# Kernel optimization log

Hardware: AMD Instinct MI355X
Metric: run time of the kernel (lower is better)

## Reference

```python
import jax, jax.numpy as jnp
import numpy as np

N_HEADS = 16

def setup_inputs() -> dict:
    key = jax.random.key(0)
    ks = jax.random.split(key, 5)
    B, N, D = 2, 2048, 1024
    return {
        "x": jax.random.normal(ks[0], (B, N, D), dtype=jnp.float32),
        "w_qkv": jax.random.normal(ks[1], (D, 3 * D), dtype=jnp.float32) * (1.0 / np.sqrt(D)),
        "b_qkv": jax.random.normal(ks[2], (3 * D,), dtype=jnp.float32) * 0.02,
        "w_out": jax.random.normal(ks[3], (D, D), dtype=jnp.float32) * (1.0 / np.sqrt(D)),
        "b_out": jax.random.normal(ks[4], (D,), dtype=jnp.float32) * 0.02,
    }

def reference(x, w_qkv, b_qkv, w_out, b_out):
    B, N, D = x.shape
    H = N_HEADS
    dk = D // H
    qkv = x @ w_qkv + b_qkv                       # (B, N, 3D)
    # NOTE: original reshapes to (B, N, H, 3*dk) then chunks -> per-head interleaved layout
    qkv = qkv.reshape(B, N, H, 3 * dk).transpose(2, 0, 1, 3)  # (H, B, N, 3*dk)
    q, k, v = jnp.split(qkv, 3, axis=-1)          # each (H, B, N, dk)
    scale = 1.0 / np.sqrt(dk).astype(np.float32)
    scores = jnp.einsum('hbnd,hbmd->hbnm', q, k) * scale  # (H, B, N, N)
    attn = jax.nn.softmax(scores, axis=-1)
    context = jnp.einsum('hbnm,hbmd->hbnd', attn, v)       # (H, B, N, dk)
    context = context.transpose(1, 2, 0, 3).reshape(B, N, D)
    attn_mean = attn.mean(axis=0).mean(axis=1)    # (B, N): mean over heads then over query dim
    out = context @ w_out + b_out
    return out, attn_mean
```

## Files before the change

### kernel.cpp

```cpp
#include <hip/hip_runtime.h>
#include <hip/hip_bf16.h>
#include <stdint.h>

#define B_ 2
#define N_ 2048
#define D_ 1024
#define H_ 16
#define DK 64

typedef __bf16 bf16x8 __attribute__((ext_vector_type(8)));
typedef short s16x4 __attribute__((ext_vector_type(4)));
typedef float f32x4 __attribute__((ext_vector_type(4)));

#define EXP2SC 0.18033688011112042f

__device__ __forceinline__ unsigned short f2bf(float f) {
    unsigned int u = __float_as_uint(f);
    u = (u + 0x7FFFu + ((u >> 16) & 1u)) >> 16;
    return (unsigned short)u;
}

__device__ __forceinline__ short2 pkbf(float a, float b) {
    __hip_bfloat162 t = __float22bfloat162_rn(float2{a, b});
    return *(short2*)&t;
}

__device__ __forceinline__ void glds16(const void* g, void* l) {
    __builtin_amdgcn_global_load_lds(
        (const __attribute__((address_space(1))) void*)g,
        (__attribute__((address_space(3))) void*)l, 16, 0, 0);
}

__global__ __launch_bounds__(256) void k_convert_x(const float* __restrict__ x,
                                                   unsigned short* __restrict__ xb, int n4) {
    int i = blockIdx.x * blockDim.x + threadIdx.x;
    int stride = gridDim.x * blockDim.x;
    const float4* x4 = (const float4*)x;
    ushort4* o4 = (ushort4*)xb;
    for (; i < n4; i += stride) {
        float4 v = x4[i];
        ushort4 o;
        o.x = f2bf(v.x); o.y = f2bf(v.y); o.z = f2bf(v.z); o.w = f2bf(v.w);
        o4[i] = o;
    }
}

__global__ __launch_bounds__(256) void k_transpose_w(const float* __restrict__ w,
                                                     unsigned short* __restrict__ wT,
                                                     int K, int C) {
    __shared__ float tile[32][33];
    int c0 = blockIdx.x * 32, k0 = blockIdx.y * 32;
    int tx = threadIdx.x, ty = threadIdx.y;
    for (int s = 0; s < 4; ++s)
        tile[ty + 8 * s][tx] = w[(size_t)(k0 + ty + 8 * s) * C + c0 + tx];
    __syncthreads();
    for (int s = 0; s < 4; ++s)
        wT[(size_t)(c0 + ty + 8 * s) * K + k0 + tx] = f2bf(tile[tx][ty + 8 * s]);
}

__global__ __launch_bounds__(256) void k_gemm_qkv(const unsigned short* __restrict__ A,
                                                  const unsigned short* __restrict__ BT,
                                                  const float* __restrict__ bias,
                                                  unsigned short* __restrict__ Cout,
                                                  int M, int Nn, int K) {
    __shared__ __attribute__((aligned(16))) unsigned short Alds[128 * 64];
    __shared__ __attribute__((aligned(16))) unsigned short Blds[128 * 64];
    int t = threadIdx.x;
    int lane = t & 63, w = t >> 6;
    int quad = lane >> 4, c = lane & 15;
    int wm = w >> 1, wn = w & 1;
    int bi = blockIdx.y, bj = blockIdx.x;
    const unsigned short* Abase = A + (size_t)(bi * 128) * K;
    const unsigned short* Bbase = BT + (size_t)(bj * 128) * K;

    f32x4 acc[4][4];
#pragma unroll
    for (int mf = 0; mf < 4; ++mf)
#pragma unroll
        for (int nf = 0; nf < 4; ++nf)
            acc[mf][nf] = (f32x4){0.f, 0.f, 0.f, 0.f};

    for (int k0 = 0; k0 < K; k0 += 64) {
        __syncthreads();
#pragma unroll
        for (int i = 0; i < 4; ++i) {
            int ch = i * 256 + t;
            int row = ch >> 3, kc = (ch & 7) ^ (row & 7);
            glds16(&Abase[(size_t)row * K + k0 + kc * 8], (char*)Alds + ch * 16);
            glds16(&Bbase[(size_t)row * K + k0 + kc * 8], (char*)Blds + ch * 16);
        }
        __syncthreads();
#pragma unroll
        for (int ks = 0; ks < 2; ++ks) {
            bf16x8 af[4], bfr[4];
#pragma unroll
            for (int mf = 0; mf < 4; ++mf)
                af[mf] = *(const bf16x8*)&Alds[(wm * 64 + mf * 16 + c) * 64 +
                                               (((ks * 4 + quad) ^ (c & 7)) * 8)];
#pragma unroll
            for (int nf = 0; nf < 4; ++nf)
                bfr[nf] = *(const bf16x8*)&Blds[(wn * 64 + nf * 16 + c) * 64 +
                                                (((ks * 4 + quad) ^ (c & 7)) * 8)];
#pragma unroll
            for (int mf = 0; mf < 4; ++mf)
#pragma unroll
                for (int nf = 0; nf < 4; ++nf)
                    acc[mf][nf] = __builtin_amdgcn_mfma_f32_16x16x32_bf16(af[mf], bfr[nf],
                                                                          acc[mf][nf], 0, 0, 0);
        }
    }

#pragma unroll
    for (int mf = 0; mf < 4; ++mf)
#pragma unroll
        for (int nf = 0; nf < 4; ++nf) {
            int j = bj * 128 + wn * 64 + nf * 16 + c;
            float bv = bias[j];
            int h = j / 192, r2 = j % 192;
            int which = r2 >> 6, d = r2 & 63;
#pragma unroll
            for (int r = 0; r < 4; ++r) {
                int i = bi * 128 + wm * 64 + mf * 16 + quad * 4 + r;
                float v = acc[mf][nf][r] + bv;
                int b = i >> 11, n = i & 2047;
                size_t dst;
                if (which < 2)
                    dst = (size_t)which * 4194304 + (((size_t)(h * 2 + b) * 2048 + n) * 64 + d);
                else
                    dst = (size_t)2 * 4194304 + (((size_t)(h * 2 + b) * 64 + d) * 2048 + n);
                Cout[dst] = f2bf(v);
            }
        }
}

__global__ __launch_bounds__(256) void k_gemm_out(const unsigned short* __restrict__ A,
                                                  const unsigned short* __restrict__ BT,
                                                  const float* __restrict__ bias,
                                                  float* __restrict__ C,
                                                  int M, int Nn, int K) {
    __shared__ __attribute__((aligned(16))) unsigned short Alds[64 * 64];
    __shared__ __attribute__((aligned(16))) unsigned short Blds[128 * 64];
    int t = threadIdx.x;
    int lane = t & 63, w = t >> 6;
    int quad = lane >> 4, c = lane & 15;
    int wm = w >> 1, wn = w & 1;
    int bi = blockIdx.y, bj = blockIdx.x;
    const unsigned short* Abase = A + (size_t)(bi * 64) * K;
    const unsigned short* Bbase = BT + (size_t)(bj * 128) * K;

    f32x4 acc[2][4];
#pragma unroll
    for (int mf = 0; mf < 2; ++mf)
#pragma unroll
        for (int nf = 0; nf < 4; ++nf)
            acc[mf][nf] = (f32x4){0.f, 0.f, 0.f, 0.f};

    for (int k0 = 0; k0 < K; k0 += 64) {
        __syncthreads();
#pragma unroll
        for (int i = 0; i < 2; ++i) {
            int ch = i * 256 + t;
            int row = ch >> 3, kc = (ch & 7) ^ (row & 7);
            glds16(&Abase[(size_t)row * K + k0 + kc * 8], (char*)Alds + ch * 16);
        }
#pragma unroll
        for (int i = 0; i < 4; ++i) {
            int ch = i * 256 + t;
            int row = ch >> 3, kc = (ch & 7) ^ (row & 7);
            glds16(&Bbase[(size_t)row * K + k0 + kc * 8], (char*)Blds + ch * 16);
        }
        __syncthreads();
#pragma unroll
        for (int ks = 0; ks < 2; ++ks) {
            bf16x8 af[2], bfr[4];
#pragma unroll
            for (int mf = 0; mf < 2; ++mf)
                af[mf] = *(const bf16x8*)&Alds[(wm * 32 + mf * 16 + c) * 64 +
                                               (((ks * 4 + quad) ^ (c & 7)) * 8)];
#pragma unroll
            for (int nf = 0; nf < 4; ++nf)
                bfr[nf] = *(const bf16x8*)&Blds[(wn * 64 + nf * 16 + c) * 64 +
                                                (((ks * 4 + quad) ^ (c & 7)) * 8)];
#pragma unroll
            for (int mf = 0; mf < 2; ++mf)
#pragma unroll
                for (int nf = 0; nf < 4; ++nf)
                    acc[mf][nf] = __builtin_amdgcn_mfma_f32_16x16x32_bf16(af[mf], bfr[nf],
                                                                          acc[mf][nf], 0, 0, 0);
        }
    }

#pragma unroll
    for (int mf = 0; mf < 2; ++mf)
#pragma unroll
        for (int nf = 0; nf < 4; ++nf) {
            int j = bj * 128 + wn * 64 + nf * 16 + c;
            float bv = bias[j];
#pragma unroll
            for (int r = 0; r < 4; ++r) {
                int i = bi * 64 + wm * 32 + mf * 16 + quad * 4 + r;
                C[(size_t)i * Nn + j] = acc[mf][nf][r] + bv;
            }
        }
}

__global__ __launch_bounds__(512) void k_attn(const unsigned short* __restrict__ Q,
                                              const unsigned short* __restrict__ Kc,
                                              const unsigned short* __restrict__ VT,
                                              unsigned short* __restrict__ ctx,
                                              float* __restrict__ lrs_out) {
    __shared__ __attribute__((aligned(16))) unsigned short lds[8192];
    unsigned short* Klds = lds;
    unsigned short* Vlds = lds + 4096;
    int t = threadIdx.x, lane = t & 63, w = t >> 6;
    int quad = lane >> 4, c = lane & 15;
    int qt = blockIdx.x, hb = blockIdx.y;
    int h = hb >> 1, b = hb & 1;
    const unsigned short* qbase = Q + (size_t)hb * 131072 + (size_t)(qt * 128 + w * 16) * 64;
    const unsigned short* kbase = Kc + (size_t)hb * 131072;
    const unsigned short* vtbase = VT + (size_t)hb * 131072;

    int srow = t >> 3, sB = t & 7;
    int sgoff = srow * 64 + ((sB ^ (srow & 7)) * 8);
    int vgoff = srow * 2048 + ((sB ^ (srow & 7)) * 8);

    bf16x8 qf[2];
#pragma unroll
    for (int ks = 0; ks < 2; ++ks)
        qf[ks] = *(const bf16x8*)&qbase[c * 64 + ks * 32 + quad * 8];

    f32x4 acc[4];
#pragma unroll
    for (int ds = 0; ds < 4; ++ds) acc[ds] = (f32x4){0.f, 0.f, 0.f, 0.f};
    float lsum = 0.f;

    for (int kb = 0; kb < 32; ++kb) {
        __syncthreads();
        glds16(&kbase[(size_t)kb * 4096 + sgoff], (char*)Klds + t * 16);
        glds16(&vtbase[(size_t)kb * 64 + vgoff], (char*)Vlds + t * 16);
        __syncthreads();

        f32x4 st[4];
#pragma unroll
        for (int ksub = 0; ksub < 4; ++ksub) st[ksub] = (f32x4){0.f, 0.f, 0.f, 0.f};
#pragma unroll
        for (int ks = 0; ks < 2; ++ks)
#pragma unroll
            for (int ksub = 0; ksub < 4; ++ksub) {
                bf16x8 kf = *(const bf16x8*)&Klds[(ksub * 16 + c) * 64 +
                                                  (((ks * 4 + quad) ^ (c & 7)) * 8)];
                st[ksub] = __builtin_amdgcn_mfma_f32_16x16x32_bf16(kf, qf[ks], st[ksub], 0, 0, 0);
            }
#pragma unroll
        for (int ksub = 0; ksub < 4; ++ksub) {
            float p0 = __builtin_amdgcn_exp2f(st[ksub][0] * EXP2SC);
            float p1 = __builtin_amdgcn_exp2f(st[ksub][1] * EXP2SC);
            float p2 = __builtin_amdgcn_exp2f(st[ksub][2] * EXP2SC);
            float p3 = __builtin_amdgcn_exp2f(st[ksub][3] * EXP2SC);
            lsum += (p0 + p1) + (p2 + p3);
            short2 lo = pkbf(p0, p1), hi = pkbf(p2, p3);
            s16x4 pf = (s16x4){lo.x, lo.y, hi.x, hi.y};
            s16x4 vf[4];
#pragma unroll
            for (int ds = 0; ds < 4; ++ds) {
                int row = ds * 16 + c;
                vf[ds] = *(const s16x4*)&Vlds[row * 64 +
                                              (((2 * ksub + (quad >> 1)) ^ (row & 7)) * 8) +
                                              (quad & 1) * 4];
            }
#pragma unroll
            for (int ds = 0; ds < 4; ++ds)
                acc[ds] = __builtin_amdgcn_mfma_f32_16x16x16bf16_1k(pf, vf[ds], acc[ds], 0, 0, 0);
        }
    }

    float v = lsum;
    v += __shfl_xor(v, 16);
    v += __shfl_xor(v, 32);
    if (lane < 16)
        lrs_out[hb * 2048 + qt * 128 + w * 16 + c] =
            -(__builtin_amdgcn_logf(v) + 15.0f);
    float linv = 1.0f / v;
    float ir[4];
#pragma unroll
    for (int r = 0; r < 4; ++r) ir[r] = __shfl(linv, quad * 4 + r);
#pragma unroll
    for (int ds = 0; ds < 4; ++ds)
#pragma unroll
        for (int r = 0; r < 4; ++r) {
            int n = qt * 128 + w * 16 + quad * 4 + r;
            ctx[((size_t)(b * 2048 + n)) * 1024 + h * 64 + ds * 16 + c] =
                f2bf(acc[ds][r] * ir[r]);
        }
}

__global__ __launch_bounds__(512) void k_amean(const unsigned short* __restrict__ Q,
                                               const unsigned short* __restrict__ Kc,
                                               const float* __restrict__ lrs,
                                               float* __restrict__ amean) {
    __shared__ __attribute__((aligned(16))) unsigned short Qlds[128 * 64];
    __shared__ float rslds[128];
    int t = threadIdx.x, lane = t & 63, w = t >> 6;
    int quad = lane >> 4, c = lane & 15;
    int kt = blockIdx.x, hb = blockIdx.y, b = hb & 1;
    const unsigned short* kbase = Kc + (size_t)hb * 131072 + (size_t)(kt * 128 + w * 16) * 64;
    const unsigned short* qbase = Q + (size_t)hb * 131072;

    bf16x8 kf[2];
#pragma unroll
    for (int ks = 0; ks < 2; ++ks)
        kf[ks] = *(const bf16x8*)&kbase[c * 64 + ks * 32 + quad * 8];

    f32x4 colacc = (f32x4){0.f, 0.f, 0.f, 0.f};

    for (int qc = 0; qc < 16; ++qc) {
        __syncthreads();
#pragma unroll
        for (int i = 0; i < 2; ++i) {
            int ch = i * 512 + t;
            int row = ch >> 3, Bs = ch & 7;
            glds16(&qbase[(size_t)qc * 8192 + row * 64 + ((Bs ^ (row & 7)) * 8)],
                   (char*)Qlds + ch * 16);
        }
        if (t < 128) rslds[t] = lrs[hb * 2048 + qc * 128 + t];
        __syncthreads();
#pragma unroll
        for (int qs = 0; qs < 8; ++qs) {
            f32x4 st = (f32x4){0.f, 0.f, 0.f, 0.f};
#pragma unroll
            for (int ks = 0; ks < 2; ++ks) {
                bf16x8 qfr = *(const bf16x8*)&Qlds[(qs * 16 + c) * 64 +
                                                   (((ks * 4 + quad) ^ (c & 7)) * 8)];
                st = __builtin_amdgcn_mfma_f32_16x16x32_bf16(kf[ks], qfr, st, 0, 0, 0);
            }
            float rv = rslds[qs * 16 + c];
#pragma unroll
            for (int r = 0; r < 4; ++r)
                colacc[r] += __builtin_amdgcn_exp2f(st[r] * EXP2SC + rv);
        }
    }
#pragma unroll
    for (int r = 0; r < 4; ++r) {
        float v = colacc[r];
        v += __shfl_xor(v, 1);
        v += __shfl_xor(v, 2);
        v += __shfl_xor(v, 4);
        v += __shfl_xor(v, 8);
        if (c == 0)
            atomicAdd(&amean[b * 2048 + kt * 128 + w * 16 + quad * 4 + r], v);
    }
}

extern "C" void kernel_launch(void* const* d_in, const int* in_sizes, int n_in,
                              void* d_out, int out_size, void* d_ws, size_t ws_size,
                              hipStream_t stream) {
    const float* x = (const float*)d_in[0];
    const float* w_qkv = (const float*)d_in[1];
    const float* b_qkv = (const float*)d_in[2];
    const float* w_out = (const float*)d_in[3];
    const float* b_out = (const float*)d_in[4];
    float* out = (float*)d_out;
    float* amean = out + 4194304;

    unsigned short* ws = (unsigned short*)d_ws;
    unsigned short* x_bf = ws;
    unsigned short* wqkvT = x_bf + 4194304;
    unsigned short* woutT = wqkvT + 3145728;
    unsigned short* q_bf = woutT + 1048576;
    unsigned short* k_bf = q_bf + 4194304;
    unsigned short* vT_bf = k_bf + 4194304;
    unsigned short* ctx_bf = vT_bf + 4194304;
    float* lrs = (float*)(ctx_bf + 4194304);

    hipMemsetAsync(amean, 0, 4096 * sizeof(float), stream);
    k_convert_x<<<2048, 256, 0, stream>>>(x, x_bf, 1048576);
    k_transpose_w<<<dim3(96, 32), dim3(32, 8), 0, stream>>>(w_qkv, wqkvT, 1024, 3072);
    k_transpose_w<<<dim3(32, 32), dim3(32, 8), 0, stream>>>(w_out, woutT, 1024, 1024);
    k_gemm_qkv<<<dim3(24, 32), 256, 0, stream>>>(x_bf, wqkvT, b_qkv, q_bf, 4096, 3072, 1024);
    k_attn<<<dim3(16, 32), 512, 0, stream>>>(q_bf, k_bf, vT_bf, ctx_bf, lrs);
    k_amean<<<dim3(16, 32), 512, 0, stream>>>(q_bf, k_bf, lrs, amean);
    k_gemm_out<<<dim3(8, 64), 256, 0, stream>>>(ctx_bf, woutT, b_out, out, 4096, 1024, 1024);
}
```

Measured before the change: 222.7 us.

## Double-buffer attention LDS loads, fuse prep kernels, fold softmax scale into Q

Merges the x conversion, both weight transposes and the amean memset into one prep kernel, removing several launches. Folds the exp2 softmax scale into Q during the QKV GEMM epilogue, so the attention and amean kernels skip one multiply per score. Double-buffers the K/V tiles in k_attn and the Q tiles in k_amean so the next tile's global-to-LDS load overlaps current compute, which doubles LDS use per block. Flattens the grid so consecutive blocks share a query/key tile index across heads, which changes block scheduling and cache locality.

```diff
diff --git a/kernel.cpp b/kernel.cpp
--- a/kernel.cpp
+++ b/kernel.cpp
@@ -31,31 +31,48 @@
         (__attribute__((address_space(3))) void*)l, 16, 0, 0);
 }
 
-__global__ __launch_bounds__(256) void k_convert_x(const float* __restrict__ x,
-                                                   unsigned short* __restrict__ xb, int n4) {
-    int i = blockIdx.x * blockDim.x + threadIdx.x;
-    int stride = gridDim.x * blockDim.x;
-    const float4* x4 = (const float4*)x;
-    ushort4* o4 = (ushort4*)xb;
-    for (; i < n4; i += stride) {
-        float4 v = x4[i];
-        ushort4 o;
-        o.x = f2bf(v.x); o.y = f2bf(v.y); o.z = f2bf(v.z); o.w = f2bf(v.w);
-        o4[i] = o;
-    }
-}
-
-__global__ __launch_bounds__(256) void k_transpose_w(const float* __restrict__ w,
-                                                     unsigned short* __restrict__ wT,
-                                                     int K, int C) {
+__global__ __launch_bounds__(256) void k_prep(const float* __restrict__ x,
+                                              unsigned short* __restrict__ xb,
+                                              const float* __restrict__ w_qkv,
+                                              unsigned short* __restrict__ wqkvT,
+                                              const float* __restrict__ w_out,
+                                              unsigned short* __restrict__ woutT,
+                                              float* __restrict__ amean) {
     __shared__ float tile[32][33];
-    int c0 = blockIdx.x * 32, k0 = blockIdx.y * 32;
-    int tx = threadIdx.x, ty = threadIdx.y;
-    for (int s = 0; s < 4; ++s)
-        tile[ty + 8 * s][tx] = w[(size_t)(k0 + ty + 8 * s) * C + c0 + tx];
-    __syncthreads();
-    for (int s = 0; s < 4; ++s)
-        wT[(size_t)(c0 + ty + 8 * s) * K + k0 + tx] = f2bf(tile[tx][ty + 8 * s]);
+    int blk = blockIdx.x, t = threadIdx.x;
+    if (blk < 1024) {
+        const float4* x4 = (const float4*)x;
+        ushort4* o4 = (ushort4*)xb;
+        int i = blk * 256 + t;
+#pragma unroll
+        for (int s = 0; s < 4; ++s, i += 262144) {
+            float4 v = x4[i];
+            ushort4 o;
+            o.x = f2bf(v.x); o.y = f2bf(v.y); o.z = f2bf(v.z); o.w = f2bf(v.w);
+            o4[i] = o;
+        }
+    } else if (blk < 4096) {
+        int idx = blk - 1024;
+        int c0 = (idx % 96) * 32, k0 = (idx / 96) * 32;
+        int tx = t & 31, ty = t >> 5;
+        for (int s = 0; s < 4; ++s)
+            tile[ty + 8 * s][tx] = w_qkv[(size_t)(k0 + ty + 8 * s) * 3072 + c0 + tx];
+        __syncthreads();
+        for (int s = 0; s < 4; ++s)
+            wqkvT[(size_t)(c0 + ty + 8 * s) * 1024 + k0 + tx] = f2bf(tile[tx][ty + 8 * s]);
+    } else if (blk < 5120) {
+        int idx = blk - 4096;
+        int c0 = (idx % 32) * 32, k0 = (idx / 32) * 32;
+        int tx = t & 31, ty = t >> 5;
+        for (int s = 0; s < 4; ++s)
+            tile[ty + 8 * s][tx] = w_out[(size_t)(k0 + ty + 8 * s) * 1024 + c0 + tx];
+        __syncthreads();
+        for (int s = 0; s < 4; ++s)
+            woutT[(size_t)(c0 + ty + 8 * s) * 1024 + k0 + tx] = f2bf(tile[tx][ty + 8 * s]);
+    } else {
+#pragma unroll
+        for (int s = 0; s < 16; ++s) amean[s * 256 + t] = 0.f;
+    }
 }
 
 __global__ __launch_bounds__(256) void k_gemm_qkv(const unsigned short* __restrict__ A,
@@ -122,6 +139,7 @@
             for (int r = 0; r < 4; ++r) {
                 int i = bi * 128 + wm * 64 + mf * 16 + quad * 4 + r;
                 float v = acc[mf][nf][r] + bv;
+                if (which == 0) v *= EXP2SC;
                 int b = i >> 11, n = i & 2047;
                 size_t dst;
                 if (which < 2)
@@ -209,12 +227,11 @@
                                               const unsigned short* __restrict__ VT,
                                               unsigned short* __restrict__ ctx,
                                               float* __restrict__ lrs_out) {
-    __shared__ __attribute__((aligned(16))) unsigned short lds[8192];
-    unsigned short* Klds = lds;
-    unsigned short* Vlds = lds + 4096;
+    __shared__ __attribute__((aligned(16))) unsigned short lds[16384];
     int t = threadIdx.x, lane = t & 63, w = t >> 6;
     int quad = lane >> 4, c = lane & 15;
-    int qt = blockIdx.x, hb = blockIdx.y;
+    int bi = blockIdx.x;
+    int hb = bi & 31, qt = bi >> 5;
     int h = hb >> 1, b = hb & 1;
     const unsigned short* qbase = Q + (size_t)hb * 131072 + (size_t)(qt * 128 + w * 16) * 64;
     const unsigned short* kbase = Kc + (size_t)hb * 131072;
@@ -229,16 +246,23 @@
     for (int ks = 0; ks < 2; ++ks)
         qf[ks] = *(const bf16x8*)&qbase[c * 64 + ks * 32 + quad * 8];
 
+    glds16(&kbase[sgoff], (char*)lds + t * 16);
+    glds16(&vtbase[vgoff], (char*)(lds + 4096) + t * 16);
+
     f32x4 acc[4];
 #pragma unroll
     for (int ds = 0; ds < 4; ++ds) acc[ds] = (f32x4){0.f, 0.f, 0.f, 0.f};
     float lsum = 0.f;
 
     for (int kb = 0; kb < 32; ++kb) {
-        __syncthreads();
-        glds16(&kbase[(size_t)kb * 4096 + sgoff], (char*)Klds + t * 16);
-        glds16(&vtbase[(size_t)kb * 64 + vgoff], (char*)Vlds + t * 16);
-        __syncthreads();
+        const unsigned short* Kb = lds + (kb & 1) * 8192;
+        const unsigned short* Vb = Kb + 4096;
+        __syncthreads();
+        if (kb < 31) {
+            unsigned short* Kn = lds + ((kb + 1) & 1) * 8192;
+            glds16(&kbase[(size_t)(kb + 1) * 4096 + sgoff], (char*)Kn + t * 16);
+            glds16(&vtbase[(size_t)(kb + 1) * 64 + vgoff], (char*)(Kn + 4096) + t * 16);
+        }
 
         f32x4 st[4];
 #pragma unroll
@@ -247,16 +271,16 @@
         for (int ks = 0; ks < 2; ++ks)
 #pragma unroll
             for (int ksub = 0; ksub < 4; ++ksub) {
-                bf16x8 kf = *(const bf16x8*)&Klds[(ksub * 16 + c) * 64 +
-                                                  (((ks * 4 + quad) ^ (c & 7)) * 8)];
+                bf16x8 kf = *(const bf16x8*)&Kb[(ksub * 16 + c) * 64 +
+                                                (((ks * 4 + quad) ^ (c & 7)) * 8)];
                 st[ksub] = __builtin_amdgcn_mfma_f32_16x16x32_bf16(kf, qf[ks], st[ksub], 0, 0, 0);
             }
 #pragma unroll
         for (int ksub = 0; ksub < 4; ++ksub) {
-            float p0 = __builtin_amdgcn_exp2f(st[ksub][0] * EXP2SC);
-            float p1 = __builtin_amdgcn_exp2f(st[ksub][1] * EXP2SC);
-            float p2 = __builtin_amdgcn_exp2f(st[ksub][2] * EXP2SC);
-            float p3 = __builtin_amdgcn_exp2f(st[ksub][3] * EXP2SC);
+            float p0 = __builtin_amdgcn_exp2f(st[ksub][0]);
+            float p1 = __builtin_amdgcn_exp2f(st[ksub][1]);
+            float p2 = __builtin_amdgcn_exp2f(st[ksub][2]);
+            float p3 = __builtin_amdgcn_exp2f(st[ksub][3]);
             lsum += (p0 + p1) + (p2 + p3);
             short2 lo = pkbf(p0, p1), hi = pkbf(p2, p3);
             s16x4 pf = (s16x4){lo.x, lo.y, hi.x, hi.y};
@@ -264,9 +288,9 @@
 #pragma unroll
             for (int ds = 0; ds < 4; ++ds) {
                 int row = ds * 16 + c;
-                vf[ds] = *(const s16x4*)&Vlds[row * 64 +
-                                              (((2 * ksub + (quad >> 1)) ^ (row & 7)) * 8) +
-                                              (quad & 1) * 4];
+                vf[ds] = *(const s16x4*)&Vb[row * 64 +
+                                            (((2 * ksub + (quad >> 1)) ^ (row & 7)) * 8) +
+                                            (quad & 1) * 4];
             }
 #pragma unroll
             for (int ds = 0; ds < 4; ++ds)
@@ -298,11 +322,12 @@
                                                const unsigned short* __restrict__ Kc,
                                                const float* __restrict__ lrs,
                                                float* __restrict__ amean) {
-    __shared__ __attribute__((aligned(16))) unsigned short Qlds[128 * 64];
-    __shared__ float rslds[128];
+    __shared__ __attribute__((aligned(16))) unsigned short Qlds[16384];
+    __shared__ float rslds[2][128];
     int t = threadIdx.x, lane = t & 63, w = t >> 6;
     int quad = lane >> 4, c = lane & 15;
-    int kt = blockIdx.x, hb = blockIdx.y, b = hb & 1;
+    int bi = blockIdx.x;
+    int hb = bi & 31, kt = bi >> 5, b = hb & 1;
     const unsigned short* kbase = Kc + (size_t)hb * 131072 + (size_t)(kt * 128 + w * 16) * 64;
     const unsigned short* qbase = Q + (size_t)hb * 131072;
 
@@ -311,32 +336,43 @@
     for (int ks = 0; ks < 2; ++ks)
         kf[ks] = *(const bf16x8*)&kbase[c * 64 + ks * 32 + quad * 8];
 
+#pragma unroll
+    for (int i = 0; i < 2; ++i) {
+        int ch = i * 512 + t;
+        int row = ch >> 3, Bs = ch & 7;
+        glds16(&qbase[row * 64 + ((Bs ^ (row & 7)) * 8)], (char*)Qlds + ch * 16);
+    }
+    if (t < 128) rslds[0][t] = lrs[hb * 2048 + t];
+
     f32x4 colacc = (f32x4){0.f, 0.f, 0.f, 0.f};
 
     for (int qc = 0; qc < 16; ++qc) {
-        __syncthreads();
-#pragma unroll
-        for (int i = 0; i < 2; ++i) {
-            int ch = i * 512 + t;
-            int row = ch >> 3, Bs = ch & 7;
-            glds16(&qbase[(size_t)qc * 8192 + row * 64 + ((Bs ^ (row & 7)) * 8)],
-                   (char*)Qlds + ch * 16);
-        }
-        if (t < 128) rslds[t] = lrs[hb * 2048 + qc * 128 + t];
-        __syncthreads();
+        const unsigned short* Qb = Qlds + (qc & 1) * 8192;
+        __syncthreads();
+        if (qc < 15) {
+            unsigned short* Qn = Qlds + ((qc + 1) & 1) * 8192;
+#pragma unroll
+            for (int i = 0; i < 2; ++i) {
+                int ch = i * 512 + t;
+                int row = ch >> 3, Bs = ch & 7;
+                glds16(&qbase[(size_t)(qc + 1) * 8192 + row * 64 + ((Bs ^ (row & 7)) * 8)],
+                       (char*)Qn + ch * 16);
+            }
+            if (t < 128) rslds[(qc + 1) & 1][t] = lrs[hb * 2048 + (qc + 1) * 128 + t];
+        }
 #pragma unroll
         for (int qs = 0; qs < 8; ++qs) {
             f32x4 st = (f32x4){0.f, 0.f, 0.f, 0.f};
 #pragma unroll
             for (int ks = 0; ks < 2; ++ks) {
-                bf16x8 qfr = *(const bf16x8*)&Qlds[(qs * 16 + c) * 64 +
-                                                   (((ks * 4 + quad) ^ (c & 7)) * 8)];
+                bf16x8 qfr = *(const bf16x8*)&Qb[(qs * 16 + c) * 64 +
+                                                 (((ks * 4 + quad) ^ (c & 7)) * 8)];
                 st = __builtin_amdgcn_mfma_f32_16x16x32_bf16(kf[ks], qfr, st, 0, 0, 0);
             }
-            float rv = rslds[qs * 16 + c];
+            float rv = rslds[qc & 1][qs * 16 + c];
 #pragma unroll
             for (int r = 0; r < 4; ++r)
-                colacc[r] += __builtin_amdgcn_exp2f(st[r] * EXP2SC + rv);
+                colacc[r] += __builtin_amdgcn_exp2f(st[r] + rv);
         }
     }
 #pragma unroll
@@ -372,12 +408,9 @@
     unsigned short* ctx_bf = vT_bf + 4194304;
     float* lrs = (float*)(ctx_bf + 4194304);
 
-    hipMemsetAsync(amean, 0, 4096 * sizeof(float), stream);
-    k_convert_x<<<2048, 256, 0, stream>>>(x, x_bf, 1048576);
-    k_transpose_w<<<dim3(96, 32), dim3(32, 8), 0, stream>>>(w_qkv, wqkvT, 1024, 3072);
-    k_transpose_w<<<dim3(32, 32), dim3(32, 8), 0, stream>>>(w_out, woutT, 1024, 1024);
+    k_prep<<<5121, 256, 0, stream>>>(x, x_bf, w_qkv, wqkvT, w_out, woutT, amean);
     k_gemm_qkv<<<dim3(24, 32), 256, 0, stream>>>(x_bf, wqkvT, b_qkv, q_bf, 4096, 3072, 1024);
-    k_attn<<<dim3(16, 32), 512, 0, stream>>>(q_bf, k_bf, vT_bf, ctx_bf, lrs);
-    k_amean<<<dim3(16, 32), 512, 0, stream>>>(q_bf, k_bf, lrs, amean);
+    k_attn<<<512, 512, 0, stream>>>(q_bf, k_bf, vT_bf, ctx_bf, lrs);
+    k_amean<<<512, 512, 0, stream>>>(q_bf, k_bf, lrs, amean);
     k_gemm_out<<<dim3(8, 64), 256, 0, stream>>>(ctx_bf, woutT, b_out, out, 4096, 1024, 1024);
 }
```

Result: no change. 223.0 us (+0.1%).
